# Kernel tuning notes

Hardware: AMD Instinct MI355X
Metric: run time of the kernel (lower is better)

## Reference

```python
import jax, jax.numpy as jnp
import numpy as np

B, N, M, KG = 2, 16384, 4096, 32
RADIUS = 0.8
CI, CL = 64, 64


def _cdist(a, b):
    # a: (B,M,3), b: (B,N,3) -> (B,M,N)
    d2 = (jnp.sum(a * a, -1)[:, :, None] + jnp.sum(b * b, -1)[:, None, :]
          - 2.0 * jnp.einsum('bmc,bnc->bmn', a, b))
    return jnp.sqrt(jnp.maximum(d2, 0.0))


def _fps(xyz, m):
    # naive sequential FPS, start index 0 (deterministic); mirrors torch loop
    b, n, _ = xyz.shape
    def step(carry, _):
        dist, far = carry
        c = jnp.take_along_axis(xyz, far[:, None, None], axis=1)  # (b,1,3)
        d = jnp.sum((xyz - c) ** 2, -1)
        dist = jnp.minimum(dist, d)
        return (dist, jnp.argmax(dist, axis=1).astype(jnp.int32)), far
    init = (jnp.full((b, n), 1e10, xyz.dtype), jnp.zeros((b,), jnp.int32))
    _, idxs = jax.lax.scan(step, init, None, length=m)
    return jnp.transpose(idxs)  # (b, m)


def setup_inputs() -> dict:
    key = jax.random.key(0)
    ks = jax.random.split(key, 32)
    def rn(i, shape, s=0.1):
        return jax.random.normal(ks[i], shape, jnp.float32) * s
    inp = {
        'xyz': jax.random.normal(ks[0], (B, N, 3), jnp.float32),
        'pts_cam': jax.random.uniform(ks[1], (B, N, 3), jnp.float32) * 80.0,
        'FI': jax.random.normal(ks[2], (B, CI, N), jnp.float32),
        'w1': rn(3, (32, 3)), 's1': jnp.ones((32,), jnp.float32), 'b1': jnp.zeros((32,), jnp.float32),
        'w2': rn(4, (32, 32)), 's2': jnp.ones((32,), jnp.float32), 'b2': jnp.zeros((32,), jnp.float32),
        'w3': rn(5, (64, 32)), 's3': jnp.ones((64,), jnp.float32), 'b3': jnp.zeros((64,), jnp.float32),
        'tw1': rn(6, (64, 1)), 'tb1': jnp.zeros((64,), jnp.float32),
        'tw2': rn(7, (64, 64)), 'tb2': jnp.zeros((64,), jnp.float32),
        'tw3': rn(8, (1, 64)), 'tb3': jnp.zeros((1,), jnp.float32),
        'gw_raw': rn(9, (64, 3)), 'gb_raw': jnp.zeros((64,), jnp.float32),
        'gw_img': rn(10, (64, 64)), 'gb_img': jnp.zeros((64,), jnp.float32),
        'gw_lid': rn(11, (64, 64)), 'gb_lid': jnp.zeros((64,), jnp.float32),
        'uw': rn(12, (1, 64)), 'ub': jnp.zeros((1,), jnp.float32),
        'vw': rn(13, (1, 64)), 'vb': jnp.zeros((1,), jnp.float32),
    }
    return inp


def reference(xyz, pts_cam, FI, w1, s1, b1, w2, s2, b2, w3, s3, b3,
              tw1, tb1, tw2, tb2, tw3, tb3,
              gw_raw, gb_raw, gw_img, gb_img, gw_lid, gb_lid, uw, ub, vw, vb):
    # --- Set abstraction: FPS + radius grouping + shared MLP + masked max ---
    idx = jax.lax.stop_gradient(_fps(xyz, M))                          # (B,M) int
    new_xyz = jnp.take_along_axis(xyz, idx[:, :, None], axis=1)        # (B,M,3)
    dists = jax.lax.stop_gradient(_cdist(new_xyz, xyz))                # (B,M,N), no_grad in torch
    negv, nidx = jax.lax.top_k(-dists, KG)                             # k nearest = argsort[:KG]
    nmask = (-negv) <= RADIUS                                          # (B,M,KG) bool
    grouped = jnp.take_along_axis(xyz[:, None], nidx[..., None], axis=2)  # (B,M,KG,3)
    g = grouped - new_xyz[:, :, None, :]                               # centered neighborhoods
    # SharedMLP2d stack (conv1x1 no-bias + BN(inference: affine) + ReLU)
    h = jax.nn.relu(jnp.einsum('bmkc,oc->bmko', g, w1) * s1 + b1)
    h = jax.nn.relu(jnp.einsum('bmkc,oc->bmko', h, w2) * s2 + b2)
    h = jax.nn.relu(jnp.einsum('bmkc,oc->bmko', h, w3) * s3 + b3)      # (B,M,KG,CL)
    h = jnp.where(nmask[..., None], h, -jnp.inf)
    FL = jnp.max(h, axis=2)                                            # (B,M,CL)
    # --- AdaptiveThresholdNet (density is constant 64/vol per the source) ---
    dens = 64.0 / (4.0 / 3.0 * 3.14159 * 1.0 ** 3)
    x = jnp.full((xyz.shape[0], 1), dens, xyz.dtype)
    t = jax.nn.relu(x @ tw1.T + tb1)
    t = jax.nn.relu(t @ tw2.T + tb2)
    t = jax.nn.sigmoid(t @ tw3.T + tb3)
    thr = 20.0 + 40.0 * t[:, 0]                                        # (B,)
    # --- DAM fusion at sampled points ---
    FI_s = jnp.take_along_axis(jnp.swapaxes(FI, 1, 2), idx[:, :, None], axis=1)  # (B,M,CI)
    fr = jax.nn.relu(new_xyz @ gw_raw.T + gb_raw)
    fi = jax.nn.relu(FI_s @ gw_img.T + gb_img)
    fl = jax.nn.relu(FL @ gw_lid.T + gb_lid)
    s = jnp.tanh(fr + fi + fl)                                         # (B,M,hid)
    wI = jax.nn.sigmoid(s @ uw.T + ub)                                 # (B,M,1)
    wL = jax.nn.sigmoid(s @ vw.T + vb)
    z = jnp.take_along_axis(pts_cam[..., 2], idx, axis=1)              # (B,M)
    near = z <= thr[:, None]
    near_f = jnp.concatenate([FL, FI_s * wI], axis=-1)                 # [FL || gated FI]
    far_f = jnp.concatenate([FI_s, FL * wL], axis=-1)                  # [FI || gated FL]
    fused = jnp.where(near[..., None], near_f, far_f)                  # (B,M,CL+CI)
    return jnp.swapaxes(fused, 1, 2)                                   # (B, CL+CI, M)
```

## Files before the change

### kernel.cpp

```cpp
#include <hip/hip_runtime.h>
#include <math.h>
#include <float.h>

#define BN   2
#define NPTS 16384
#define MPTS 4096
#define KGN  32
#define CIN  64
#define CLN  64

__device__ __forceinline__ float exadd(float a, float b) {
#pragma clang fp contract(off)
    float r = a + b; return r;
}
__device__ __forceinline__ float exsub(float a, float b) {
#pragma clang fp contract(off)
    float r = a - b; return r;
}
__device__ __forceinline__ float exmul(float a, float b) {
#pragma clang fp contract(off)
    float r = a * b; return r;
}

__device__ __forceinline__ float wave_sum64(float v) {
#pragma unroll
    for (int off = 1; off < 64; off <<= 1) v += __shfl_xor(v, off);
    return v;
}

__global__ __launch_bounds__(256) void prep_kernel(const float* __restrict__ xyz,
                                                   float4* __restrict__ pts4) {
    const int i = blockIdx.x * 256 + threadIdx.x;
    const float x = xyz[3 * i + 0];
    const float y = xyz[3 * i + 1];
    const float z = xyz[3 * i + 2];
    const float sb = exadd(exadd(exmul(x, x), exmul(y, y)), exmul(z, z));
    pts4[i] = make_float4(x, y, z, sb);
}

__global__ __attribute__((amdgpu_waves_per_eu(4, 4)))
__launch_bounds__(1024) void fps_kernel(const float4* __restrict__ P4,
                                        int* __restrict__ out_idx) {
    const int b = blockIdx.x;
    const int t = threadIdx.x;
    const float4* P = P4 + (size_t)b * NPTS;

    float px[16], py[16], pz[16], dist[16];
#pragma unroll
    for (int i = 0; i < 16; ++i) {
        float4 a = P[t * 16 + i];
        px[i] = a.x;
        py[i] = a.y;
        pz[i] = a.z;
        dist[i] = 1e10f;
    }
#pragma unroll
    for (int i = 0; i < 16; ++i) {
        asm volatile("" : "+v"(px[i]), "+v"(py[i]), "+v"(pz[i]));
    }

    __shared__ float sc[3];
    __shared__ int   sfar;
    __shared__ unsigned long long swave[16];
    __shared__ unsigned long long swin;

    if (t == 0) { sc[0] = px[0]; sc[1] = py[0]; sc[2] = pz[0]; sfar = 0; }
    __syncthreads();

    for (int m = 0; m < MPTS; ++m) {
        float cx = sc[0], cy = sc[1], cz = sc[2];
        if (t == 0) out_idx[b * MPTS + m] = sfar;

        float lmax = -1.0f;
#pragma unroll
        for (int i = 0; i < 16; ++i) {
            float dx = exsub(px[i], cx);
            float dy = exsub(py[i], cy);
            float dz = exsub(pz[i], cz);
            float d  = exadd(exadd(exmul(dx, dx), exmul(dy, dy)), exmul(dz, dz));
            float nd = fminf(dist[i], d);
            dist[i] = nd;
            lmax = fmaxf(lmax, nd);
        }
        unsigned long long pk =
            ((unsigned long long)__float_as_uint(lmax) << 32) |
            (unsigned long long)(0xFFFFFFFFu - (unsigned)t);
#pragma unroll
        for (int off = 32; off > 0; off >>= 1) {
            unsigned long long o = __shfl_xor(pk, off);
            pk = (o > pk) ? o : pk;
        }
        if ((t & 63) == 0) swave[t >> 6] = pk;
        __syncthreads();
        if (t == 0) {
            unsigned long long w = swave[0];
#pragma unroll
            for (int i = 1; i < 16; ++i) { unsigned long long o = swave[i]; if (o > w) w = o; }
            swin = w;
        }
        __syncthreads();
        unsigned long long w = swin;
        int wtid = (int)(0xFFFFFFFFu - (unsigned)(w & 0xFFFFFFFFull));
        unsigned vbits = (unsigned)(w >> 32);
        if (t == wtid) {
            int sel = 0; float wx = 0.f, wy = 0.f, wz = 0.f;
#pragma unroll
            for (int i = 15; i >= 0; --i) {
                if (__float_as_uint(dist[i]) == vbits) { sel = i; wx = px[i]; wy = py[i]; wz = pz[i]; }
            }
            sfar = t * 16 + sel;
            sc[0] = wx; sc[1] = wy; sc[2] = wz;
        }
        __syncthreads();
    }
}

__global__ __launch_bounds__(256) void knn_kernel(const float4* __restrict__ pts4,
                                                  const int* __restrict__ fps_idx,
                                                  float* __restrict__ newxyz,
                                                  int* __restrict__ nn_idx,
                                                  float* __restrict__ nn_key) {
    const int lane = threadIdx.x & 63;
    const int g    = blockIdx.x * 4 + (threadIdx.x >> 6);
    const int b    = g >> 12;
    const float4* P = pts4 + (size_t)b * NPTS;

    const int far = fps_idx[g];
    const float4 C = P[far];
    if (lane == 0) {
        newxyz[g * 3 + 0] = C.x;
        newxyz[g * 3 + 1] = C.y;
        newxyz[g * 3 + 2] = C.z;
    }
    const float sa = C.w;

    float skey = FLT_MAX;
    int   sidx = 0;

    for (int it = 0; it < NPTS / 64; ++it) {
        const int j = it * 64 + lane;
        const float4 Q = P[j];
        const float dot = exadd(exadd(exmul(C.x, Q.x), exmul(C.y, Q.y)), exmul(C.z, Q.z));
        const float d2  = exsub(exadd(sa, Q.w), exadd(dot, dot));
        const float dk  = fmaxf(d2, 0.0f);
        const float tk = __shfl(skey, 31);
        const int   ti = __shfl(sidx, 31);
        const bool pass = (sqrtf(dk) <= 0.8f) &&
                          ((dk < tk) || (dk == tk && j < ti));
        unsigned long long mask = __ballot(pass);
        while (mask) {
            const int src = __ffsll(mask) - 1;
            mask &= mask - 1;
            const float ck = __shfl(dk, src);
            const int   cj = it * 64 + src;
            const bool less = (skey < ck) || (skey == ck && sidx < cj);
            const int p = __popcll(__ballot(less));
            if (p < 32) {
                const float upk = __shfl_up(skey, 1);
                const int   upi = __shfl_up(sidx, 1);
                if (lane < 32) {
                    if (lane == p)     { skey = ck;  sidx = cj; }
                    else if (lane > p) { skey = upk; sidx = upi; }
                }
            }
        }
    }
    if (lane < KGN) {
        nn_idx[(size_t)g * KGN + lane] = sidx;
        nn_key[(size_t)g * KGN + lane] = skey;
    }
}

__global__ __attribute__((amdgpu_waves_per_eu(4, 4)))
__launch_bounds__(256) void mlp_kernel(const float* __restrict__ xyz,
                                       const float* __restrict__ w1, const float* __restrict__ s1, const float* __restrict__ b1,
                                       const float* __restrict__ w2, const float* __restrict__ s2, const float* __restrict__ b2,
                                       const float* __restrict__ w3, const float* __restrict__ s3, const float* __restrict__ b3,
                                       const float* __restrict__ newxyz,
                                       const int* __restrict__ nn_idx,
                                       const float* __restrict__ nn_key,
                                       float* __restrict__ FLout) {
    __shared__ float W1[96], S1[32], B1[32];
    __shared__ float W2[1024], S2[32], B2[32];
    __shared__ float W3[2048], S3[64], B3[64];
    const int tid = threadIdx.x;
    for (int i = tid; i < 96; i += 256)   W1[i] = w1[i];
    for (int i = tid; i < 32; i += 256) { S1[i] = s1[i]; B1[i] = b1[i]; S2[i] = s2[i]; B2[i] = b2[i]; }
    for (int i = tid; i < 1024; i += 256) W2[i] = w2[i];
    for (int i = tid; i < 2048; i += 256) W3[i] = w3[i];
    for (int i = tid; i < 64; i += 256) { S3[i] = s3[i]; B3[i] = b3[i]; }
    __syncthreads();

    const int n  = tid & 31;
    const int g  = blockIdx.x * 8 + (tid >> 5);
    const int b  = g >> 12;
    const size_t base = (size_t)g * KGN + n;
    const int   nj = nn_idx[base];
    const float nk = nn_key[base];

    const float* X = xyz + (size_t)b * NPTS * 3;
    const float gx = X[nj * 3 + 0] - newxyz[g * 3 + 0];
    const float gy = X[nj * 3 + 1] - newxyz[g * 3 + 1];
    const float gz = X[nj * 3 + 2] - newxyz[g * 3 + 2];

    float h1[32];
#pragma unroll
    for (int o = 0; o < 32; ++o) {
        float a = gx * W1[o * 3 + 0] + gy * W1[o * 3 + 1] + gz * W1[o * 3 + 2];
        h1[o] = fmaxf(a * S1[o] + B1[o], 0.0f);
    }
    float h2[32];
#pragma unroll
    for (int o = 0; o < 32; ++o) {
        float a = 0.0f;
#pragma unroll
        for (int k = 0; k < 32; ++k) a += h1[k] * W2[o * 32 + k];
        h2[o] = fmaxf(a * S2[o] + B2[o], 0.0f);
    }
    const bool valid = (sqrtf(nk) <= 0.8f);

    for (int o = 0; o < 64; ++o) {
        float a = 0.0f;
#pragma unroll
        for (int k = 0; k < 32; ++k) a += h2[k] * W3[o * 32 + k];
        float v = fmaxf(a * S3[o] + B3[o], 0.0f);
        v = valid ? v : -INFINITY;
#pragma unroll
        for (int off = 1; off < 32; off <<= 1) v = fmaxf(v, __shfl_xor(v, off));
        if (n == (o & 31)) FLout[(size_t)g * CLN + o] = v;
    }
}

__global__ __launch_bounds__(256) void fuse_kernel(const float* __restrict__ pts_cam,
                                                   const float* __restrict__ FIn,
                                                   const float* __restrict__ tw1, const float* __restrict__ tb1,
                                                   const float* __restrict__ tw2, const float* __restrict__ tb2,
                                                   const float* __restrict__ tw3, const float* __restrict__ tb3,
                                                   const float* __restrict__ gw_raw, const float* __restrict__ gb_raw,
                                                   const float* __restrict__ gw_img, const float* __restrict__ gb_img,
                                                   const float* __restrict__ gw_lid, const float* __restrict__ gb_lid,
                                                   const float* __restrict__ uw, const float* __restrict__ ub,
                                                   const float* __restrict__ vw, const float* __restrict__ vb,
                                                   const int* __restrict__ fps_idx,
                                                   const float* __restrict__ newxyz,
                                                   const float* __restrict__ FLin,
                                                   float* __restrict__ out) {
    __shared__ float WIm[4096], WLi[4096], WT2[4096];
    const int tid = threadIdx.x;
    for (int i = tid; i < 4096; i += 256) {
        int c = i >> 6, k = i & 63;
        WIm[k * 64 + c] = gw_img[i];
        WLi[k * 64 + c] = gw_lid[i];
        WT2[k * 64 + c] = tw2[i];
    }
    __syncthreads();

    const int lane = tid & 63;
    const int g    = blockIdx.x * 4 + (tid >> 6);
    const int b    = g >> 12;
    const int m    = g & (MPTS - 1);
    const int far  = fps_idx[g];

    const float fi_in = FIn[((size_t)(b * CIN + lane)) * NPTS + far];
    const float fl_in = FLin[(size_t)g * CLN + lane];
    const float nx = newxyz[g * 3 + 0], ny = newxyz[g * 3 + 1], nz = newxyz[g * 3 + 2];

    float fr = fmaxf(nx * gw_raw[lane * 3 + 0] + ny * gw_raw[lane * 3 + 1] +
                     nz * gw_raw[lane * 3 + 2] + gb_raw[lane], 0.0f);

    float ai = gb_img[lane], al = gb_lid[lane];
#pragma unroll 8
    for (int k = 0; k < 64; ++k) {
        float vi = __shfl(fi_in, k);
        float vl = __shfl(fl_in, k);
        ai += vi * WIm[k * 64 + lane];
        al += vl * WLi[k * 64 + lane];
    }
    const float s = tanhf(fr + fmaxf(ai, 0.0f) + fmaxf(al, 0.0f));

    const float dens = (float)(64.0 / (4.0 / 3.0 * 3.14159 * 1.0));
    float t1 = fmaxf(dens * tw1[lane] + tb1[lane], 0.0f);
    float a2 = tb2[lane];
#pragma unroll 8
    for (int k = 0; k < 64; ++k) a2 += __shfl(t1, k) * WT2[k * 64 + lane];
    float t2 = fmaxf(a2, 0.0f);
    float a3 = wave_sum64(t2 * tw3[lane]) + tb3[0];
    float thr = 20.0f + 40.0f * (1.0f / (1.0f + expf(-a3)));

    float aI = wave_sum64(s * uw[lane]) + ub[0];
    float aL = wave_sum64(s * vw[lane]) + vb[0];
    float wIv = 1.0f / (1.0f + expf(-aI));
    float wLv = 1.0f / (1.0f + expf(-aL));

    const float z = pts_cam[((size_t)b * NPTS + far) * 3 + 2];
    const bool near = (z <= thr);

    const size_t o1 = ((size_t)(b * 128 + lane)) * MPTS + m;
    out[o1]                       = near ? fl_in        : fi_in;
    out[o1 + (size_t)64 * MPTS]   = near ? fi_in * wIv  : fl_in * wLv;
}

extern "C" void kernel_launch(void* const* d_in, const int* in_sizes, int n_in,
                              void* d_out, int out_size, void* d_ws, size_t ws_size,
                              hipStream_t stream) {
    const float* xyz     = (const float*)d_in[0];
    const float* pts_cam = (const float*)d_in[1];
    const float* FI      = (const float*)d_in[2];
    const float* w1 = (const float*)d_in[3];
    const float* s1 = (const float*)d_in[4];
    const float* b1 = (const float*)d_in[5];
    const float* w2 = (const float*)d_in[6];
    const float* s2 = (const float*)d_in[7];
    const float* b2 = (const float*)d_in[8];
    const float* w3 = (const float*)d_in[9];
    const float* s3 = (const float*)d_in[10];
    const float* b3 = (const float*)d_in[11];
    const float* tw1 = (const float*)d_in[12];
    const float* tb1 = (const float*)d_in[13];
    const float* tw2 = (const float*)d_in[14];
    const float* tb2 = (const float*)d_in[15];
    const float* tw3 = (const float*)d_in[16];
    const float* tb3 = (const float*)d_in[17];
    const float* gw_raw = (const float*)d_in[18];
    const float* gb_raw = (const float*)d_in[19];
    const float* gw_img = (const float*)d_in[20];
    const float* gb_img = (const float*)d_in[21];
    const float* gw_lid = (const float*)d_in[22];
    const float* gb_lid = (const float*)d_in[23];
    const float* uw = (const float*)d_in[24];
    const float* ub = (const float*)d_in[25];
    const float* vw = (const float*)d_in[26];
    const float* vb = (const float*)d_in[27];
    float* out = (float*)d_out;

    char* ws = (char*)d_ws;
    int*    ws_idx    = (int*)   (ws + 0);
    float*  ws_newxyz = (float*) (ws + 32768);
    float4* ws_pts4   = (float4*)(ws + 131072);
    float*  ws_FL     = (float*) (ws + 131072);
    int*    ws_nnidx  = (int*)   (ws + 2228224);
    float*  ws_nnkey  = (float*) (ws + 3276800);
    (void)ws_size; (void)in_sizes; (void)n_in; (void)out_size;

    prep_kernel<<<(BN * NPTS) / 256, 256, 0, stream>>>(xyz, ws_pts4);
    fps_kernel<<<BN, 1024, 0, stream>>>(ws_pts4, ws_idx);
    knn_kernel<<<2048, 256, 0, stream>>>(ws_pts4, ws_idx, ws_newxyz, ws_nnidx, ws_nnkey);
    mlp_kernel<<<1024, 256, 0, stream>>>(xyz, w1, s1, b1, w2, s2, b2, w3, s3, b3,
                                         ws_newxyz, ws_nnidx, ws_nnkey, ws_FL);
    fuse_kernel<<<2048, 256, 0, stream>>>(pts_cam, FI, tw1, tb1, tw2, tb2, tw3, tb3,
                                          gw_raw, gb_raw, gw_img, gb_img, gw_lid, gb_lid,
                                          uw, ub, vw, vb, ws_idx, ws_newxyz, ws_FL, out);
}
```

Baseline: 7.308 ms.

## Cut FPS iteration to one barrier with redundant per-wave reduction and global centroid load

Each FPS step now carries the point index in the packed key, so no winner-thread lookup is needed. Every wave reads all 16 wave maxima from a double-buffered shared array and reduces them itself with shuffles. The new centroid is then loaded straight from global memory. This drops two of the three block barriers per iteration and the serial reduction on thread 0, at the cost of a dependent global (likely cached) load each step. The waves_per_eu attribute is also replaced with launch_bounds(1024,1).

```diff
diff --git a/kernel.cpp b/kernel.cpp
--- a/kernel.cpp
+++ b/kernel.cpp
@@ -38,9 +38,8 @@
     pts4[i] = make_float4(x, y, z, sb);
 }
 
-__global__ __attribute__((amdgpu_waves_per_eu(4, 4)))
-__launch_bounds__(1024) void fps_kernel(const float4* __restrict__ P4,
-                                        int* __restrict__ out_idx) {
+__global__ __launch_bounds__(1024, 1) void fps_kernel(const float4* __restrict__ P4,
+                                                      int* __restrict__ out_idx) {
     const int b = blockIdx.x;
     const int t = threadIdx.x;
     const float4* P = P4 + (size_t)b * NPTS;
@@ -54,24 +53,22 @@
         pz[i] = a.z;
         dist[i] = 1e10f;
     }
-#pragma unroll
-    for (int i = 0; i < 16; ++i) {
-        asm volatile("" : "+v"(px[i]), "+v"(py[i]), "+v"(pz[i]));
-    }
-
-    __shared__ float sc[3];
-    __shared__ int   sfar;
-    __shared__ unsigned long long swave[16];
-    __shared__ unsigned long long swin;
-
-    if (t == 0) { sc[0] = px[0]; sc[1] = py[0]; sc[2] = pz[0]; sfar = 0; }
-    __syncthreads();
+
+    __shared__ unsigned long long swave[2][16];
+
+    int pidx = 0;
+    float4 cen = P[0];
 
     for (int m = 0; m < MPTS; ++m) {
-        float cx = sc[0], cy = sc[1], cz = sc[2];
-        if (t == 0) out_idx[b * MPTS + m] = sfar;
-
+#pragma unroll
+        for (int i = 0; i < 16; ++i) {
+            asm volatile("" : "+v"(px[i]), "+v"(py[i]), "+v"(pz[i]));
+        }
+        if (t == 0) out_idx[b * MPTS + m] = pidx;
+
+        const float cx = cen.x, cy = cen.y, cz = cen.z;
         float lmax = -1.0f;
+        int   argp = 0;
 #pragma unroll
         for (int i = 0; i < 16; ++i) {
             float dx = exsub(px[i], cx);
@@ -80,38 +77,26 @@
             float d  = exadd(exadd(exmul(dx, dx), exmul(dy, dy)), exmul(dz, dz));
             float nd = fminf(dist[i], d);
             dist[i] = nd;
-            lmax = fmaxf(lmax, nd);
+            if (nd > lmax) { lmax = nd; argp = t * 16 + i; }
         }
         unsigned long long pk =
             ((unsigned long long)__float_as_uint(lmax) << 32) |
-            (unsigned long long)(0xFFFFFFFFu - (unsigned)t);
+            (unsigned long long)(0xFFFFFFFFu - (unsigned)argp);
 #pragma unroll
         for (int off = 32; off > 0; off >>= 1) {
             unsigned long long o = __shfl_xor(pk, off);
             pk = (o > pk) ? o : pk;
         }
-        if ((t & 63) == 0) swave[t >> 6] = pk;
+        if ((t & 63) == 0) swave[m & 1][t >> 6] = pk;
         __syncthreads();
-        if (t == 0) {
-            unsigned long long w = swave[0];
-#pragma unroll
-            for (int i = 1; i < 16; ++i) { unsigned long long o = swave[i]; if (o > w) w = o; }
-            swin = w;
-        }
-        __syncthreads();
-        unsigned long long w = swin;
-        int wtid = (int)(0xFFFFFFFFu - (unsigned)(w & 0xFFFFFFFFull));
-        unsigned vbits = (unsigned)(w >> 32);
-        if (t == wtid) {
-            int sel = 0; float wx = 0.f, wy = 0.f, wz = 0.f;
-#pragma unroll
-            for (int i = 15; i >= 0; --i) {
-                if (__float_as_uint(dist[i]) == vbits) { sel = i; wx = px[i]; wy = py[i]; wz = pz[i]; }
-            }
-            sfar = t * 16 + sel;
-            sc[0] = wx; sc[1] = wy; sc[2] = wz;
-        }
-        __syncthreads();
+        unsigned long long w = swave[m & 1][t & 15];
+#pragma unroll
+        for (int off = 1; off < 16; off <<= 1) {
+            unsigned long long o = __shfl_xor(w, off);
+            w = (o > w) ? o : w;
+        }
+        pidx = (int)(0xFFFFFFFFu - (unsigned)(w & 0xFFFFFFFFull));
+        cen = P[pidx];
     }
 }
 
```

Measured after the change: 9.612 ms. 31.5% more time.
